# Kernel tuning notes

Measured on AMD Instinct MI355X. Metric: run time of the kernel, lower is better.

## Reference

```python
import jax, jax.numpy as jnp
import numpy as np

L, S, N, E, H = 2048, 2048, 4, 1024, 16
D = E // H  # head_dim = 64


def setup_inputs() -> dict:
    key = jax.random.key(0)
    ks = jax.random.split(key, 7)
    scale = 1.0 / np.sqrt(E)
    return {
        "query": jax.random.normal(ks[0], (L, N, E), jnp.float32),
        "key": jax.random.normal(ks[1], (S, N, E), jnp.float32),
        "value": jax.random.normal(ks[2], (S, N, E), jnp.float32),
        "in_proj_w": jax.random.normal(ks[3], (3 * E, E), jnp.float32) * scale,
        "in_proj_b": jax.random.normal(ks[4], (3 * E,), jnp.float32) * 0.01,
        "out_proj_w": jax.random.normal(ks[5], (E, E), jnp.float32) * scale * 0.25,
        "out_proj_b": jax.random.normal(ks[6], (E,), jnp.float32) * 0.01,
    }


def reference(query, key, value, in_proj_w, in_proj_b, out_proj_w, out_proj_b):
    # Split packed in-projection into q/k/v parts (torch layout: [3E, E]).
    wq, wk, wv = in_proj_w[:E], in_proj_w[E:2 * E], in_proj_w[2 * E:]
    bq, bk, bv = in_proj_b[:E], in_proj_b[E:2 * E], in_proj_b[2 * E:]

    def proj(x, w, b):  # (T,N,E) -> (N,H,T,D)
        y = jnp.einsum('tne,fe->tnf', x, w) + b
        T = x.shape[0]
        return y.reshape(T, N, H, D).transpose(1, 2, 0, 3)

    q = proj(query, wq, bq) * (1.0 / np.sqrt(D))  # scale queries
    k = proj(key, wk, bk)
    v = proj(value, wv, bv)

    scores = jnp.einsum('nhld,nhsd->nhls', q, k)  # (N,H,L,S)
    attn = jax.nn.softmax(scores, axis=-1)
    ctx = jnp.einsum('nhls,nhsd->nhld', attn, v)  # (N,H,L,D)
    ctx = ctx.transpose(2, 0, 1, 3).reshape(L, N, E)  # (L,N,E)

    out = jnp.einsum('lne,fe->lnf', ctx, out_proj_w) + out_proj_b
    attn_weights = attn.mean(axis=1)  # (N,L,S), averaged over heads (torch default)
    return out, attn_weights
```

## Files before the change

### kernel.cpp

```cpp
#include <hip/hip_runtime.h>
#include <hip/hip_bf16.h>

#define L_ 2048
#define S_ 2048
#define NB 4
#define E_ 1024
#define H_ 16
#define D_ 64
#define LDT 72

typedef __attribute__((ext_vector_type(8))) short bf16x8;
typedef __attribute__((ext_vector_type(4))) float f32x4;

__device__ __forceinline__ short f2bf(float f) {
  union { float f; unsigned u; } v; v.f = f;
  unsigned r = v.u + 0x7FFFu + ((v.u >> 16) & 1u);
  return (short)(r >> 16);
}

__global__ void k_convert(const float* __restrict__ wi, const float* __restrict__ wo,
                          short* __restrict__ wqkv, short* __restrict__ wout) {
  const int n1 = 3 * E_ * E_ / 4;
  const int n2 = E_ * E_ / 4;
  const int stride = gridDim.x * blockDim.x;
  for (int i = blockIdx.x * blockDim.x + threadIdx.x; i < n1 + n2; i += stride) {
    const float4* s; short* d; int j;
    if (i < n1) { s = (const float4*)wi; d = wqkv; j = i; }
    else        { s = (const float4*)wo; d = wout; j = i - n1; }
    float4 v = s[j];
    short4 o = make_short4(f2bf(v.x), f2bf(v.y), f2bf(v.z), f2bf(v.w));
    *(short4*)&d[(size_t)j * 4] = o;
  }
}

__global__ __launch_bounds__(256) void k_qkv(
    const float* __restrict__ qin, const float* __restrict__ kin, const float* __restrict__ vin,
    const short* __restrict__ wbf, const float* __restrict__ bias,
    short* __restrict__ qh, short* __restrict__ kh, short* __restrict__ vh) {
  __shared__ short As[128 * LDT];
  __shared__ short Bs[128 * LDT];
  const int bm = blockIdx.x;
  const int fbase = blockIdx.y * 128;
  const int mat = fbase >> 10;
  const float* __restrict__ A = (mat == 0) ? qin : (mat == 1) ? kin : vin;
  short* __restrict__ dst = (mat == 0) ? qh : (mat == 1) ? kh : vh;
  const float scale = (mat == 0) ? 0.125f * 1.44269504088896f : 1.0f;
  const int tid = threadIdx.x;
  const int lane = tid & 63, wid = tid >> 6;
  const int wr = wid >> 1, wc = wid & 1;
  const int lr = lane & 15, lk = lane >> 4;
  f32x4 acc[4][4] = {};

  for (int kb = 0; kb < E_; kb += 64) {
#pragma unroll
    for (int i = 0; i < 8; ++i) {
      int f4 = i * 256 + tid;
      int row = f4 >> 4, k4 = f4 & 15;
      float4 v = *(const float4*)&A[(size_t)(bm * 128 + row) * E_ + kb + k4 * 4];
      short4 o = make_short4(f2bf(v.x), f2bf(v.y), f2bf(v.z), f2bf(v.w));
      *(short4*)&As[row * LDT + k4 * 4] = o;
    }
#pragma unroll
    for (int i = 0; i < 4; ++i) {
      int e8 = i * 256 + tid;
      int row = e8 >> 3, k8 = e8 & 7;
      int4 v = *(const int4*)&wbf[(size_t)(fbase + row) * E_ + kb + k8 * 8];
      *(int4*)&Bs[row * LDT + k8 * 8] = v;
    }
    __syncthreads();
#pragma unroll
    for (int kk = 0; kk < 2; ++kk) {
      bf16x8 a[4], b[4];
#pragma unroll
      for (int fi = 0; fi < 4; ++fi)
        a[fi] = *(const bf16x8*)&As[(wr * 64 + fi * 16 + lr) * LDT + kk * 32 + lk * 8];
#pragma unroll
      for (int ci = 0; ci < 4; ++ci)
        b[ci] = *(const bf16x8*)&Bs[(wc * 64 + ci * 16 + lr) * LDT + kk * 32 + lk * 8];
#pragma unroll
      for (int fi = 0; fi < 4; ++fi)
#pragma unroll
        for (int ci = 0; ci < 4; ++ci)
          acc[fi][ci] = __builtin_amdgcn_mfma_f32_16x16x32_bf16(a[fi], b[ci], acc[fi][ci], 0, 0, 0);
    }
    __syncthreads();
  }
#pragma unroll
  for (int ci = 0; ci < 4; ++ci) {
    const int fg = fbase + wc * 64 + ci * 16 + lr;
    const float b = bias[fg];
    const int col = fg & 1023;
    const int h = col >> 6, d = col & 63;
#pragma unroll
    for (int fi = 0; fi < 4; ++fi)
#pragma unroll
      for (int j = 0; j < 4; ++j) {
        int m = bm * 128 + wr * 64 + fi * 16 + lk * 4 + j;
        int t = m >> 2, n = m & 3;
        float vv = (acc[fi][ci][j] + b) * scale;
        dst[(((size_t)(n * H_ + h) * L_ + t) << 6) + d] = f2bf(vv);
      }
  }
}

__global__ __launch_bounds__(256) void k_vtrans(const short* __restrict__ vh,
                                                short* __restrict__ vt) {
  __shared__ short t[64][LDT];
  const int nh = blockIdx.y;
  const int tb = blockIdx.x;
  const int tid = threadIdx.x;
  const short* __restrict__ src = vh + ((size_t)nh * L_ + tb * 64) * D_;
  short* __restrict__ dst = vt + (size_t)nh * D_ * S_ + tb * 64;
#pragma unroll
  for (int i = 0; i < 2; ++i) {
    int v = i * 256 + tid;
    int r = v >> 3, c8 = v & 7;
    *(bf16x8*)&t[r][c8 * 8] = *(const bf16x8*)&src[(size_t)r * D_ + c8 * 8];
  }
  __syncthreads();
#pragma unroll
  for (int i = 0; i < 2; ++i) {
    int v = i * 256 + tid;
    int d = v >> 3, t8 = v & 7;
    bf16x8 o;
#pragma unroll
    for (int e = 0; e < 8; ++e) o[e] = t[t8 * 8 + e][d];
    *(bf16x8*)&dst[(size_t)d * S_ + t8 * 8] = o;
  }
}

__global__ __launch_bounds__(256) void k_stats(
    const short* __restrict__ qh, const short* __restrict__ kh, float* __restrict__ rl) {
  const int nh = blockIdx.y;
  const int qt = blockIdx.x;
  const short* __restrict__ Q = qh + (size_t)nh * L_ * D_;
  const short* __restrict__ K = kh + (size_t)nh * S_ * D_;
  const int tid = threadIdx.x;
  const int lane = tid & 63, wid = tid >> 6;
  const int lr = lane & 15, lk = lane >> 4;
  const int rbase = qt * 128 + wid * 32;
  bf16x8 a[2][2];
#pragma unroll
  for (int ri = 0; ri < 2; ++ri)
#pragma unroll
    for (int kk = 0; kk < 2; ++kk)
      a[ri][kk] = *(const bf16x8*)&Q[(size_t)(rbase + ri * 16 + lr) * D_ + kk * 32 + lk * 8];
  float ssum[2][4] = {};
  for (int st = 0; st < S_; st += 64) {
    f32x4 acc[2][4] = {};
#pragma unroll
    for (int ci = 0; ci < 4; ++ci) {
      bf16x8 b0 = *(const bf16x8*)&K[(size_t)(st + ci * 16 + lr) * D_ + lk * 8];
      bf16x8 b1 = *(const bf16x8*)&K[(size_t)(st + ci * 16 + lr) * D_ + 32 + lk * 8];
#pragma unroll
      for (int ri = 0; ri < 2; ++ri) {
        acc[ri][ci] = __builtin_amdgcn_mfma_f32_16x16x32_bf16(a[ri][0], b0, acc[ri][ci], 0, 0, 0);
        acc[ri][ci] = __builtin_amdgcn_mfma_f32_16x16x32_bf16(a[ri][1], b1, acc[ri][ci], 0, 0, 0);
      }
    }
#pragma unroll
    for (int ri = 0; ri < 2; ++ri)
#pragma unroll
      for (int j = 0; j < 4; ++j) {
        float s = __builtin_amdgcn_exp2f(acc[ri][0][j]) + __builtin_amdgcn_exp2f(acc[ri][1][j]) +
                  __builtin_amdgcn_exp2f(acc[ri][2][j]) + __builtin_amdgcn_exp2f(acc[ri][3][j]);
        s += __shfl_xor(s, 1);
        s += __shfl_xor(s, 2);
        s += __shfl_xor(s, 4);
        s += __shfl_xor(s, 8);
        ssum[ri][j] += s;
      }
  }
  if (lr == 0) {
#pragma unroll
    for (int ri = 0; ri < 2; ++ri)
#pragma unroll
      for (int j = 0; j < 4; ++j)
        rl[(size_t)nh * L_ + rbase + ri * 16 + lk * 4 + j] = 1.0f / ssum[ri][j];
  }
}

__global__ __launch_bounds__(1024) void k_attn(
    const short* __restrict__ qh, const short* __restrict__ kh, const short* __restrict__ vt,
    const float* __restrict__ rl, float* __restrict__ attnw, short* __restrict__ ctx) {
  __shared__ short psl[16][32 * 40];
  const int n = blockIdx.y, qt = blockIdx.x;
  const int tid = threadIdx.x;
  const int h = tid >> 6, lane = tid & 63;
  const int lr = lane & 15, lk = lane >> 4;
  const size_t nh = (size_t)(n * H_ + h);
  const short* __restrict__ Q = qh + nh * L_ * D_;
  const short* __restrict__ K = kh + nh * S_ * D_;
  const short* __restrict__ VT = vt + nh * D_ * S_;
  const int rbase = qt * 32;
  bf16x8 qf[2][2];
#pragma unroll
  for (int li = 0; li < 2; ++li)
#pragma unroll
    for (int kk = 0; kk < 2; ++kk)
      qf[li][kk] = *(const bf16x8*)&Q[(size_t)(rbase + li * 16 + lr) * D_ + kk * 32 + lk * 8];
  float rls[2];
#pragma unroll
  for (int li = 0; li < 2; ++li)
    rls[li] = rl[nh * L_ + rbase + li * 16 + lr];
  f32x4 cacc[2][4] = {};
  const int mrow = tid >> 4, mcp = tid & 15;
  float* awp = attnw + ((size_t)n * L_ + rbase + mrow) * S_;

  for (int st = 0; st < S_; st += 32) {
    f32x4 sacc[2][2] = {};
#pragma unroll
    for (int si = 0; si < 2; ++si) {
      bf16x8 k0 = *(const bf16x8*)&K[(size_t)(st + si * 16 + lr) * D_ + lk * 8];
      bf16x8 k1 = *(const bf16x8*)&K[(size_t)(st + si * 16 + lr) * D_ + 32 + lk * 8];
#pragma unroll
      for (int li = 0; li < 2; ++li) {
        sacc[si][li] = __builtin_amdgcn_mfma_f32_16x16x32_bf16(k0, qf[li][0], sacc[si][li], 0, 0, 0);
        sacc[si][li] = __builtin_amdgcn_mfma_f32_16x16x32_bf16(k1, qf[li][1], sacc[si][li], 0, 0, 0);
      }
    }
    bf16x8 vb[4];
#pragma unroll
    for (int ci = 0; ci < 4; ++ci)
      vb[ci] = *(const bf16x8*)&VT[(size_t)(ci * 16 + lr) * S_ + st + lk * 8];
#pragma unroll
    for (int si = 0; si < 2; ++si)
#pragma unroll
      for (int li = 0; li < 2; ++li) {
        short4 pk;
        pk.x = f2bf(__builtin_amdgcn_exp2f(sacc[si][li][0]) * rls[li]);
        pk.y = f2bf(__builtin_amdgcn_exp2f(sacc[si][li][1]) * rls[li]);
        pk.z = f2bf(__builtin_amdgcn_exp2f(sacc[si][li][2]) * rls[li]);
        pk.w = f2bf(__builtin_amdgcn_exp2f(sacc[si][li][3]) * rls[li]);
        *(short4*)&psl[h][(li * 16 + lr) * 40 + si * 16 + lk * 4] = pk;
      }
    bf16x8 pa[2];
#pragma unroll
    for (int li = 0; li < 2; ++li)
      pa[li] = *(const bf16x8*)&psl[h][(li * 16 + lr) * 40 + lk * 8];
#pragma unroll
    for (int ci = 0; ci < 4; ++ci)
#pragma unroll
      for (int li = 0; li < 2; ++li)
        cacc[li][ci] = __builtin_amdgcn_mfma_f32_16x16x32_bf16(pa[li], vb[ci], cacc[li][ci], 0, 0, 0);
    __syncthreads();
    if (tid < 512) {
      float s0 = 0.f, s1 = 0.f;
#pragma unroll
      for (int w = 0; w < 16; ++w) {
        unsigned u = *(const unsigned*)&psl[w][mrow * 40 + mcp * 2];
        union { unsigned u; float f; } a, b;
        a.u = u << 16; b.u = u & 0xFFFF0000u;
        s0 += a.f; s1 += b.f;
      }
      float2 o = make_float2(s0 * 0.0625f, s1 * 0.0625f);
      *(float2*)&awp[st + mcp * 2] = o;
    }
    __syncthreads();
  }
#pragma unroll
  for (int li = 0; li < 2; ++li)
#pragma unroll
    for (int ci = 0; ci < 4; ++ci)
#pragma unroll
      for (int j = 0; j < 4; ++j) {
        int row = rbase + li * 16 + lk * 4 + j;
        int d = ci * 16 + lr;
        ctx[((size_t)row * NB + n) * E_ + h * 64 + d] = f2bf(cacc[li][ci][j]);
      }
}

__global__ __launch_bounds__(256) void k_out(
    const short* __restrict__ ctxb, const short* __restrict__ wbf,
    const float* __restrict__ bias, float* __restrict__ out) {
  __shared__ short As[128 * LDT];
  __shared__ short Bs[128 * LDT];
  const int bm = blockIdx.x, bn = blockIdx.y;
  const int tid = threadIdx.x;
  const int lane = tid & 63, wid = tid >> 6;
  const int wr = wid >> 1, wc = wid & 1;
  const int lr = lane & 15, lk = lane >> 4;
  f32x4 acc[4][4] = {};
  for (int kb = 0; kb < E_; kb += 64) {
#pragma unroll
    for (int i = 0; i < 4; ++i) {
      int e8 = i * 256 + tid;
      int row = e8 >> 3, k8 = e8 & 7;
      int4 va = *(const int4*)&ctxb[(size_t)(bm * 128 + row) * E_ + kb + k8 * 8];
      *(int4*)&As[row * LDT + k8 * 8] = va;
      int4 vb = *(const int4*)&wbf[(size_t)(bn * 128 + row) * E_ + kb + k8 * 8];
      *(int4*)&Bs[row * LDT + k8 * 8] = vb;
    }
    __syncthreads();
#pragma unroll
    for (int kk = 0; kk < 2; ++kk) {
      bf16x8 a[4], b[4];
#pragma unroll
      for (int fi = 0; fi < 4; ++fi)
        a[fi] = *(const bf16x8*)&As[(wr * 64 + fi * 16 + lr) * LDT + kk * 32 + lk * 8];
#pragma unroll
      for (int ci = 0; ci < 4; ++ci)
        b[ci] = *(const bf16x8*)&Bs[(wc * 64 + ci * 16 + lr) * LDT + kk * 32 + lk * 8];
#pragma unroll
      for (int fi = 0; fi < 4; ++fi)
#pragma unroll
        for (int ci = 0; ci < 4; ++ci)
          acc[fi][ci] = __builtin_amdgcn_mfma_f32_16x16x32_bf16(a[fi], b[ci], acc[fi][ci], 0, 0, 0);
    }
    __syncthreads();
  }
#pragma unroll
  for (int ci = 0; ci < 4; ++ci) {
    int col = bn * 128 + wc * 64 + ci * 16 + lr;
    float b = bias[col];
#pragma unroll
    for (int fi = 0; fi < 4; ++fi)
#pragma unroll
      for (int j = 0; j < 4; ++j) {
        int m = bm * 128 + wr * 64 + fi * 16 + lk * 4 + j;
        out[(size_t)m * E_ + col] = acc[fi][ci][j] + b;
      }
  }
}

extern "C" void kernel_launch(void* const* d_in, const int* in_sizes, int n_in,
                              void* d_out, int out_size, void* d_ws, size_t ws_size,
                              hipStream_t stream) {
  const float* qin = (const float*)d_in[0];
  const float* kin = (const float*)d_in[1];
  const float* vin = (const float*)d_in[2];
  const float* wi  = (const float*)d_in[3];
  const float* bi  = (const float*)d_in[4];
  const float* wo  = (const float*)d_in[5];
  const float* bo  = (const float*)d_in[6];
  float* out = (float*)d_out;
  float* attnw = out + (size_t)L_ * NB * E_;

  short* wqkv = (short*)d_ws;
  short* wout = wqkv + (size_t)3 * E_ * E_;
  short* qh = wout + (size_t)E_ * E_;
  short* kh = qh + (size_t)NB * L_ * E_;
  short* vh = kh + (size_t)NB * L_ * E_;
  short* vt = vh + (size_t)NB * L_ * E_;
  float* rl = (float*)(vt + (size_t)NB * L_ * E_);
  short* ctx = (short*)(rl + (size_t)NB * H_ * L_);

  k_convert<<<1024, 256, 0, stream>>>(wi, wo, wqkv, wout);
  k_qkv<<<dim3(64, 24), 256, 0, stream>>>(qin, kin, vin, wqkv, bi, qh, kh, vh);
  k_vtrans<<<dim3(32, 64), 256, 0, stream>>>(vh, vt);
  k_stats<<<dim3(16, 64), 256, 0, stream>>>(qh, kh, rl);
  k_attn<<<dim3(64, 4), 1024, 0, stream>>>(qh, kh, vt, rl, attnw, ctx);
  k_out<<<dim3(64, 8), 256, 0, stream>>>(ctx, wout, bo, out);
}
```

Before: 511.5 us.

## Halve attention query tile, double-buffer probability smem, and block V-transpose layout

The attention kernel now processes 16 query rows per block instead of 32, doubling the grid to 512 blocks, and sets a launch-bounds occupancy hint. The shared probability buffer is double-buffered so the head-averaged attention-weight reduction for the previous tile overlaps the current tile's compute, which removes one barrier per iteration. The transposed V is stored in 32-key blocks so each tile's V loads are contiguous. The trade-off is less reuse of K and V loads per block and twice as much K/V traffic overall.

```diff
diff --git a/kernel.cpp b/kernel.cpp
--- a/kernel.cpp
+++ b/kernel.cpp
@@ -110,7 +110,7 @@
   const int tb = blockIdx.x;
   const int tid = threadIdx.x;
   const short* __restrict__ src = vh + ((size_t)nh * L_ + tb * 64) * D_;
-  short* __restrict__ dst = vt + (size_t)nh * D_ * S_ + tb * 64;
+  short* __restrict__ dst = vt + (size_t)nh * S_ * D_;
 #pragma unroll
   for (int i = 0; i < 2; ++i) {
     int v = i * 256 + tid;
@@ -125,7 +125,8 @@
     bf16x8 o;
 #pragma unroll
     for (int e = 0; e < 8; ++e) o[e] = t[t8 * 8 + e][d];
-    *(bf16x8*)&dst[(size_t)d * S_ + t8 * 8] = o;
+    int sb = tb * 2 + (t8 >> 2);
+    *(bf16x8*)&dst[(size_t)sb * (D_ * 32) + d * 32 + (t8 & 3) * 8] = o;
   }
 }
 
@@ -180,10 +181,10 @@
   }
 }
 
-__global__ __launch_bounds__(1024) void k_attn(
+__global__ __launch_bounds__(1024, 8) void k_attn(
     const short* __restrict__ qh, const short* __restrict__ kh, const short* __restrict__ vt,
     const float* __restrict__ rl, float* __restrict__ attnw, short* __restrict__ ctx) {
-  __shared__ short psl[16][32 * 40];
+  __shared__ short psl[2][16][16 * 40];
   const int n = blockIdx.y, qt = blockIdx.x;
   const int tid = threadIdx.x;
   const int h = tid >> 6, lane = tid & 63;
@@ -191,83 +192,77 @@
   const size_t nh = (size_t)(n * H_ + h);
   const short* __restrict__ Q = qh + nh * L_ * D_;
   const short* __restrict__ K = kh + nh * S_ * D_;
-  const short* __restrict__ VT = vt + nh * D_ * S_;
-  const int rbase = qt * 32;
-  bf16x8 qf[2][2];
-#pragma unroll
-  for (int li = 0; li < 2; ++li)
-#pragma unroll
-    for (int kk = 0; kk < 2; ++kk)
-      qf[li][kk] = *(const bf16x8*)&Q[(size_t)(rbase + li * 16 + lr) * D_ + kk * 32 + lk * 8];
-  float rls[2];
-#pragma unroll
-  for (int li = 0; li < 2; ++li)
-    rls[li] = rl[nh * L_ + rbase + li * 16 + lr];
-  f32x4 cacc[2][4] = {};
-  const int mrow = tid >> 4, mcp = tid & 15;
-  float* awp = attnw + ((size_t)n * L_ + rbase + mrow) * S_;
-
-  for (int st = 0; st < S_; st += 32) {
-    f32x4 sacc[2][2] = {};
+  const short* __restrict__ VT = vt + nh * S_ * D_;
+  const int rbase = qt * 16;
+  bf16x8 qf[2];
+#pragma unroll
+  for (int kk = 0; kk < 2; ++kk)
+    qf[kk] = *(const bf16x8*)&Q[(size_t)(rbase + lr) * D_ + kk * 32 + lk * 8];
+  const float rls = rl[nh * L_ + rbase + lr];
+  f32x4 cacc[4] = {};
+  const int mrow = (tid & 255) >> 4, mcp = tid & 15;
+  float* awp = attnw + ((size_t)n * L_ + rbase + mrow) * S_ + mcp * 2;
+
+  int p = 0;
+  for (int st = 0; st < S_; st += 32, p ^= 1) {
+    bf16x8 vb[4];
+#pragma unroll
+    for (int ci = 0; ci < 4; ++ci)
+      vb[ci] = *(const bf16x8*)&VT[(size_t)(st >> 5) * (D_ * 32) + (ci * 16 + lr) * 32 + lk * 8];
+    bf16x8 k0 = *(const bf16x8*)&K[(size_t)(st + lr) * D_ + lk * 8];
+    bf16x8 k1 = *(const bf16x8*)&K[(size_t)(st + lr) * D_ + 32 + lk * 8];
+    bf16x8 k2 = *(const bf16x8*)&K[(size_t)(st + 16 + lr) * D_ + lk * 8];
+    bf16x8 k3 = *(const bf16x8*)&K[(size_t)(st + 16 + lr) * D_ + 32 + lk * 8];
+    f32x4 sacc[2] = {};
+    sacc[0] = __builtin_amdgcn_mfma_f32_16x16x32_bf16(k0, qf[0], sacc[0], 0, 0, 0);
+    sacc[0] = __builtin_amdgcn_mfma_f32_16x16x32_bf16(k1, qf[1], sacc[0], 0, 0, 0);
+    sacc[1] = __builtin_amdgcn_mfma_f32_16x16x32_bf16(k2, qf[0], sacc[1], 0, 0, 0);
+    sacc[1] = __builtin_amdgcn_mfma_f32_16x16x32_bf16(k3, qf[1], sacc[1], 0, 0, 0);
 #pragma unroll
     for (int si = 0; si < 2; ++si) {
-      bf16x8 k0 = *(const bf16x8*)&K[(size_t)(st + si * 16 + lr) * D_ + lk * 8];
-      bf16x8 k1 = *(const bf16x8*)&K[(size_t)(st + si * 16 + lr) * D_ + 32 + lk * 8];
-#pragma unroll
-      for (int li = 0; li < 2; ++li) {
-        sacc[si][li] = __builtin_amdgcn_mfma_f32_16x16x32_bf16(k0, qf[li][0], sacc[si][li], 0, 0, 0);
-        sacc[si][li] = __builtin_amdgcn_mfma_f32_16x16x32_bf16(k1, qf[li][1], sacc[si][li], 0, 0, 0);
-      }
-    }
-    bf16x8 vb[4];
+      short4 pk;
+      pk.x = f2bf(__builtin_amdgcn_exp2f(sacc[si][0]) * rls);
+      pk.y = f2bf(__builtin_amdgcn_exp2f(sacc[si][1]) * rls);
+      pk.z = f2bf(__builtin_amdgcn_exp2f(sacc[si][2]) * rls);
+      pk.w = f2bf(__builtin_amdgcn_exp2f(sacc[si][3]) * rls);
+      *(short4*)&psl[p][h][lr * 40 + si * 16 + lk * 4] = pk;
+    }
+    bf16x8 pa = *(const bf16x8*)&psl[p][h][lr * 40 + lk * 8];
 #pragma unroll
     for (int ci = 0; ci < 4; ++ci)
-      vb[ci] = *(const bf16x8*)&VT[(size_t)(ci * 16 + lr) * S_ + st + lk * 8];
-#pragma unroll
-    for (int si = 0; si < 2; ++si)
-#pragma unroll
-      for (int li = 0; li < 2; ++li) {
-        short4 pk;
-        pk.x = f2bf(__builtin_amdgcn_exp2f(sacc[si][li][0]) * rls[li]);
-        pk.y = f2bf(__builtin_amdgcn_exp2f(sacc[si][li][1]) * rls[li]);
-        pk.z = f2bf(__builtin_amdgcn_exp2f(sacc[si][li][2]) * rls[li]);
-        pk.w = f2bf(__builtin_amdgcn_exp2f(sacc[si][li][3]) * rls[li]);
-        *(short4*)&psl[h][(li * 16 + lr) * 40 + si * 16 + lk * 4] = pk;
-      }
-    bf16x8 pa[2];
-#pragma unroll
-    for (int li = 0; li < 2; ++li)
-      pa[li] = *(const bf16x8*)&psl[h][(li * 16 + lr) * 40 + lk * 8];
-#pragma unroll
-    for (int ci = 0; ci < 4; ++ci)
-#pragma unroll
-      for (int li = 0; li < 2; ++li)
-        cacc[li][ci] = __builtin_amdgcn_mfma_f32_16x16x32_bf16(pa[li], vb[ci], cacc[li][ci], 0, 0, 0);
-    __syncthreads();
-    if (tid < 512) {
+      cacc[ci] = __builtin_amdgcn_mfma_f32_16x16x32_bf16(pa, vb[ci], cacc[ci], 0, 0, 0);
+    if (st > 0 && tid < 256) {
       float s0 = 0.f, s1 = 0.f;
 #pragma unroll
       for (int w = 0; w < 16; ++w) {
-        unsigned u = *(const unsigned*)&psl[w][mrow * 40 + mcp * 2];
+        unsigned u = *(const unsigned*)&psl[p ^ 1][w][mrow * 40 + mcp * 2];
         union { unsigned u; float f; } a, b;
         a.u = u << 16; b.u = u & 0xFFFF0000u;
         s0 += a.f; s1 += b.f;
       }
-      float2 o = make_float2(s0 * 0.0625f, s1 * 0.0625f);
-      *(float2*)&awp[st + mcp * 2] = o;
-    }
-    __syncthreads();
-  }
-#pragma unroll
-  for (int li = 0; li < 2; ++li)
-#pragma unroll
-    for (int ci = 0; ci < 4; ++ci)
-#pragma unroll
-      for (int j = 0; j < 4; ++j) {
-        int row = rbase + li * 16 + lk * 4 + j;
-        int d = ci * 16 + lr;
-        ctx[((size_t)row * NB + n) * E_ + h * 64 + d] = f2bf(cacc[li][ci][j]);
-      }
+      *(float2*)&awp[st - 32] = make_float2(s0 * 0.0625f, s1 * 0.0625f);
+    }
+    __syncthreads();
+  }
+  if (tid < 256) {
+    float s0 = 0.f, s1 = 0.f;
+#pragma unroll
+    for (int w = 0; w < 16; ++w) {
+      unsigned u = *(const unsigned*)&psl[p ^ 1][w][mrow * 40 + mcp * 2];
+      union { unsigned u; float f; } a, b;
+      a.u = u << 16; b.u = u & 0xFFFF0000u;
+      s0 += a.f; s1 += b.f;
+    }
+    *(float2*)&awp[S_ - 32] = make_float2(s0 * 0.0625f, s1 * 0.0625f);
+  }
+#pragma unroll
+  for (int ci = 0; ci < 4; ++ci)
+#pragma unroll
+    for (int j = 0; j < 4; ++j) {
+      int row = rbase + lk * 4 + j;
+      int d = ci * 16 + lr;
+      ctx[((size_t)row * NB + n) * E_ + h * 64 + d] = f2bf(cacc[ci][j]);
+    }
 }
 
 __global__ __launch_bounds__(256) void k_out(
@@ -349,6 +344,6 @@
   k_qkv<<<dim3(64, 24), 256, 0, stream>>>(qin, kin, vin, wqkv, bi, qh, kh, vh);
   k_vtrans<<<dim3(32, 64), 256, 0, stream>>>(vh, vt);
   k_stats<<<dim3(16, 64), 256, 0, stream>>>(qh, kh, rl);
-  k_attn<<<dim3(64, 4), 1024, 0, stream>>>(qh, kh, vt, rl, attnw, ctx);
+  k_attn<<<dim3(128, 4), 1024, 0, stream>>>(qh, kh, vt, rl, attnw, ctx);
   k_out<<<dim3(64, 8), 256, 0, stream>>>(ctx, wout, bo, out);
 }
```

After: 612.1 us. 1.2x slower.

## Restructure attention kernel: two heads per wave, 64-wide S tiles, swizzled LDS

Applied to the files above, without the earlier changes.

The attention kernel now runs 512 threads, with each wave handling two heads, and steps through S in tiles of 64 instead of 32. This halves the number of block barriers and head-mean reduction passes. V^T is stored in 32-column blocks so each wave's V loads are contiguous. The probability slab in LDS uses an XOR swizzle to avoid bank conflicts, and the head-average writes float4 instead of float2. The trade-off is fewer waves per block and higher register pressure from the doubled accumulators and fragments.

```diff
diff --git a/kernel.cpp b/kernel.cpp
--- a/kernel.cpp
+++ b/kernel.cpp
@@ -17,6 +17,17 @@
   unsigned r = v.u + 0x7FFFu + ((v.u >> 16) & 1u);
   return (short)(r >> 16);
 }
+__device__ __forceinline__ float bf2f(short s) {
+  union { unsigned u; float f; } v; v.u = ((unsigned)(unsigned short)s) << 16;
+  return v.f;
+}
+
+#define LGKM_BARRIER() do {                                   \
+    asm volatile("s_waitcnt lgkmcnt(0)" ::: "memory");        \
+    __builtin_amdgcn_sched_barrier(0);                        \
+    __builtin_amdgcn_s_barrier();                             \
+    __builtin_amdgcn_sched_barrier(0);                        \
+  } while (0)
 
 __global__ void k_convert(const float* __restrict__ wi, const float* __restrict__ wo,
                           short* __restrict__ wqkv, short* __restrict__ wout) {
@@ -110,7 +121,7 @@
   const int tb = blockIdx.x;
   const int tid = threadIdx.x;
   const short* __restrict__ src = vh + ((size_t)nh * L_ + tb * 64) * D_;
-  short* __restrict__ dst = vt + (size_t)nh * D_ * S_ + tb * 64;
+  short* __restrict__ dst = vt + (size_t)nh * S_ * D_;
 #pragma unroll
   for (int i = 0; i < 2; ++i) {
     int v = i * 256 + tid;
@@ -125,7 +136,8 @@
     bf16x8 o;
 #pragma unroll
     for (int e = 0; e < 8; ++e) o[e] = t[t8 * 8 + e][d];
-    *(bf16x8*)&dst[(size_t)d * S_ + t8 * 8] = o;
+    int sb = tb * 2 + (t8 >> 2);
+    *(bf16x8*)&dst[(size_t)sb * (D_ * 32) + d * 32 + (t8 & 3) * 8] = o;
   }
 }
 
@@ -180,94 +192,112 @@
   }
 }
 
-__global__ __launch_bounds__(1024) void k_attn(
+__global__ __launch_bounds__(512) void k_attn(
     const short* __restrict__ qh, const short* __restrict__ kh, const short* __restrict__ vt,
     const float* __restrict__ rl, float* __restrict__ attnw, short* __restrict__ ctx) {
-  __shared__ short psl[16][32 * 40];
+  __shared__ short psl[16][32][64];
   const int n = blockIdx.y, qt = blockIdx.x;
   const int tid = threadIdx.x;
-  const int h = tid >> 6, lane = tid & 63;
+  const int wid = tid >> 6, lane = tid & 63;
   const int lr = lane & 15, lk = lane >> 4;
-  const size_t nh = (size_t)(n * H_ + h);
-  const short* __restrict__ Q = qh + nh * L_ * D_;
-  const short* __restrict__ K = kh + nh * S_ * D_;
-  const short* __restrict__ VT = vt + nh * D_ * S_;
   const int rbase = qt * 32;
-  bf16x8 qf[2][2];
-#pragma unroll
-  for (int li = 0; li < 2; ++li)
-#pragma unroll
-    for (int kk = 0; kk < 2; ++kk)
-      qf[li][kk] = *(const bf16x8*)&Q[(size_t)(rbase + li * 16 + lr) * D_ + kk * 32 + lk * 8];
-  float rls[2];
-#pragma unroll
-  for (int li = 0; li < 2; ++li)
-    rls[li] = rl[nh * L_ + rbase + li * 16 + lr];
-  f32x4 cacc[2][4] = {};
-  const int mrow = tid >> 4, mcp = tid & 15;
-  float* awp = attnw + ((size_t)n * L_ + rbase + mrow) * S_;
-
-  for (int st = 0; st < S_; st += 32) {
-    f32x4 sacc[2][2] = {};
-#pragma unroll
-    for (int si = 0; si < 2; ++si) {
-      bf16x8 k0 = *(const bf16x8*)&K[(size_t)(st + si * 16 + lr) * D_ + lk * 8];
-      bf16x8 k1 = *(const bf16x8*)&K[(size_t)(st + si * 16 + lr) * D_ + 32 + lk * 8];
-#pragma unroll
-      for (int li = 0; li < 2; ++li) {
-        sacc[si][li] = __builtin_amdgcn_mfma_f32_16x16x32_bf16(k0, qf[li][0], sacc[si][li], 0, 0, 0);
-        sacc[si][li] = __builtin_amdgcn_mfma_f32_16x16x32_bf16(k1, qf[li][1], sacc[si][li], 0, 0, 0);
-      }
-    }
-    bf16x8 vb[4];
-#pragma unroll
-    for (int ci = 0; ci < 4; ++ci)
-      vb[ci] = *(const bf16x8*)&VT[(size_t)(ci * 16 + lr) * S_ + st + lk * 8];
-#pragma unroll
-    for (int si = 0; si < 2; ++si)
-#pragma unroll
-      for (int li = 0; li < 2; ++li) {
-        short4 pk;
-        pk.x = f2bf(__builtin_amdgcn_exp2f(sacc[si][li][0]) * rls[li]);
-        pk.y = f2bf(__builtin_amdgcn_exp2f(sacc[si][li][1]) * rls[li]);
-        pk.z = f2bf(__builtin_amdgcn_exp2f(sacc[si][li][2]) * rls[li]);
-        pk.w = f2bf(__builtin_amdgcn_exp2f(sacc[si][li][3]) * rls[li]);
-        *(short4*)&psl[h][(li * 16 + lr) * 40 + si * 16 + lk * 4] = pk;
-      }
-    bf16x8 pa[2];
+
+  const size_t nh0 = (size_t)(n * H_ + wid * 2);
+  const short* __restrict__ Kp[2] = { kh + nh0 * S_ * D_, kh + (nh0 + 1) * S_ * D_ };
+  const short* __restrict__ Vp[2] = { vt + nh0 * S_ * D_, vt + (nh0 + 1) * S_ * D_ };
+  char* slab[2] = { (char*)&psl[wid * 2][0][0], (char*)&psl[wid * 2 + 1][0][0] };
+
+  bf16x8 qf[2][2][2];
+  float rls[2][2];
+  f32x4 cacc[2][2][4] = {};
+#pragma unroll
+  for (int hp = 0; hp < 2; ++hp) {
+    const short* Q = qh + (nh0 + hp) * L_ * D_;
+#pragma unroll
+    for (int li = 0; li < 2; ++li) {
+#pragma unroll
+      for (int kk = 0; kk < 2; ++kk)
+        qf[hp][li][kk] = *(const bf16x8*)&Q[(size_t)(rbase + li * 16 + lr) * D_ + kk * 32 + lk * 8];
+      rls[hp][li] = rl[(nh0 + hp) * L_ + rbase + li * 16 + lr];
+    }
+  }
+  const int mrow = tid >> 4, mc4 = (tid & 15) * 4;
+  float* awp = attnw + ((size_t)n * L_ + rbase + mrow) * S_ + mc4;
+  const int mswz = (mc4 * 2) ^ ((mrow & 7) << 4);
+
+  for (int st = 0; st < S_; st += 64) {
+#pragma unroll
+    for (int hp = 0; hp < 2; ++hp) {
+      const short* __restrict__ K = Kp[hp];
+      const short* __restrict__ VT = Vp[hp];
+      bf16x8 kf[4][2], vb[4][2];
+#pragma unroll
+      for (int u = 0; u < 4; ++u)
+#pragma unroll
+        for (int kk = 0; kk < 2; ++kk)
+          kf[u][kk] = *(const bf16x8*)&K[(size_t)(st + u * 16 + lr) * D_ + kk * 32 + lk * 8];
+#pragma unroll
+      for (int b = 0; b < 2; ++b) {
+        const size_t sb = (size_t)((st >> 5) + b) * (D_ * 32);
+#pragma unroll
+        for (int ci = 0; ci < 4; ++ci)
+          vb[ci][b] = *(const bf16x8*)&VT[sb + (ci * 16 + lr) * 32 + lk * 8];
+      }
+      f32x4 sacc[4][2] = {};
+#pragma unroll
+      for (int u = 0; u < 4; ++u)
+#pragma unroll
+        for (int li = 0; li < 2; ++li) {
+          sacc[u][li] = __builtin_amdgcn_mfma_f32_16x16x32_bf16(kf[u][0], qf[hp][li][0], sacc[u][li], 0, 0, 0);
+          sacc[u][li] = __builtin_amdgcn_mfma_f32_16x16x32_bf16(kf[u][1], qf[hp][li][1], sacc[u][li], 0, 0, 0);
+        }
+#pragma unroll
+      for (int u = 0; u < 4; ++u)
+#pragma unroll
+        for (int li = 0; li < 2; ++li) {
+          short4 pk;
+          pk.x = f2bf(__builtin_amdgcn_exp2f(sacc[u][li][0]) * rls[hp][li]);
+          pk.y = f2bf(__builtin_amdgcn_exp2f(sacc[u][li][1]) * rls[hp][li]);
+          pk.z = f2bf(__builtin_amdgcn_exp2f(sacc[u][li][2]) * rls[hp][li]);
+          pk.w = f2bf(__builtin_amdgcn_exp2f(sacc[u][li][3]) * rls[hp][li]);
+          const int row = li * 16 + lr;
+          *(short4*)(slab[hp] + row * 128 + ((u * 32 + lk * 8) ^ ((row & 7) << 4))) = pk;
+        }
+#pragma unroll
+      for (int b = 0; b < 2; ++b)
+#pragma unroll
+        for (int li = 0; li < 2; ++li) {
+          const int row = li * 16 + lr;
+          bf16x8 pa = *(const bf16x8*)(slab[hp] + row * 128 + ((b * 64 + lk * 16) ^ ((row & 7) << 4)));
+#pragma unroll
+          for (int ci = 0; ci < 4; ++ci)
+            cacc[hp][li][ci] = __builtin_amdgcn_mfma_f32_16x16x32_bf16(pa, vb[ci][b], cacc[hp][li][ci], 0, 0, 0);
+        }
+    }
+    LGKM_BARRIER();
+    {
+      float s0 = 0.f, s1 = 0.f, s2 = 0.f, s3 = 0.f;
+#pragma unroll
+      for (int hh = 0; hh < 16; ++hh) {
+        short4 m = *(const short4*)((char*)psl + hh * 4096 + mrow * 128 + mswz);
+        s0 += bf2f(m.x); s1 += bf2f(m.y); s2 += bf2f(m.z); s3 += bf2f(m.w);
+      }
+      *(float4*)&awp[st] = make_float4(s0 * 0.0625f, s1 * 0.0625f, s2 * 0.0625f, s3 * 0.0625f);
+    }
+    LGKM_BARRIER();
+  }
+#pragma unroll
+  for (int hp = 0; hp < 2; ++hp)
 #pragma unroll
     for (int li = 0; li < 2; ++li)
-      pa[li] = *(const bf16x8*)&psl[h][(li * 16 + lr) * 40 + lk * 8];
-#pragma unroll
-    for (int ci = 0; ci < 4; ++ci)
-#pragma unroll
-      for (int li = 0; li < 2; ++li)
-        cacc[li][ci] = __builtin_amdgcn_mfma_f32_16x16x32_bf16(pa[li], vb[ci], cacc[li][ci], 0, 0, 0);
-    __syncthreads();
-    if (tid < 512) {
-      float s0 = 0.f, s1 = 0.f;
-#pragma unroll
-      for (int w = 0; w < 16; ++w) {
-        unsigned u = *(const unsigned*)&psl[w][mrow * 40 + mcp * 2];
-        union { unsigned u; float f; } a, b;
-        a.u = u << 16; b.u = u & 0xFFFF0000u;
-        s0 += a.f; s1 += b.f;
-      }
-      float2 o = make_float2(s0 * 0.0625f, s1 * 0.0625f);
-      *(float2*)&awp[st + mcp * 2] = o;
-    }
-    __syncthreads();
-  }
-#pragma unroll
-  for (int li = 0; li < 2; ++li)
-#pragma unroll
-    for (int ci = 0; ci < 4; ++ci)
-#pragma unroll
-      for (int j = 0; j < 4; ++j) {
-        int row = rbase + li * 16 + lk * 4 + j;
-        int d = ci * 16 + lr;
-        ctx[((size_t)row * NB + n) * E_ + h * 64 + d] = f2bf(cacc[li][ci][j]);
-      }
+#pragma unroll
+      for (int ci = 0; ci < 4; ++ci)
+#pragma unroll
+        for (int j = 0; j < 4; ++j) {
+          int row = rbase + li * 16 + lk * 4 + j;
+          int d = ci * 16 + lr;
+          ctx[((size_t)row * NB + n) * E_ + (wid * 2 + hp) * 64 + d] = f2bf(cacc[hp][li][ci][j]);
+        }
 }
 
 __global__ __launch_bounds__(256) void k_out(
@@ -349,6 +379,6 @@
   k_qkv<<<dim3(64, 24), 256, 0, stream>>>(qin, kin, vin, wqkv, bi, qh, kh, vh);
   k_vtrans<<<dim3(32, 64), 256, 0, stream>>>(vh, vt);
   k_stats<<<dim3(16, 64), 256, 0, stream>>>(qh, kh, rl);
-  k_attn<<<dim3(64, 4), 1024, 0, stream>>>(qh, kh, vt, rl, attnw, ctx);
+  k_attn<<<dim3(64, 4), 512, 0, stream>>>(qh, kh, vt, rl, attnw, ctx);
   k_out<<<dim3(64, 8), 256, 0, stream>>>(ctx, wout, bo, out);
 }
```

Result: faster. 474.5 us (-7.2%).
